# Performance work log

Measured on AMD Instinct MI355X. Metric: run time of the kernel, lower is better.

## Reference

```python
import jax, jax.numpy as jnp
import numpy as np

COORD = 5.0
NOOBJ = 0.5


def _reflat(x):
    # torch: flatten(x.transpose(0,1), start_dim=1).transpose(0,1) -> [B*S*S, C]
    C = x.shape[1]
    return jnp.moveaxis(x, 1, -1).reshape(-1, C)


def setup_inputs() -> dict:
    key = jax.random.key(0)
    k1, k2 = jax.random.split(key)
    B, C, S = 256, 25, 64
    inp = jax.random.uniform(k1, (B, C, S, S), dtype=jnp.float32)
    tgt = jax.random.uniform(k2, (B, C, S, S), dtype=jnp.float32)
    return {"input": inp, "target": tgt}


def _iou(b1, b2, blocks):
    # vectorized, detached IoU between predicted and target boxes, per row
    b1 = jax.lax.stop_gradient(b1)
    b2 = jax.lax.stop_gradient(b2)
    c1 = b1[:, :2] / blocks
    c2 = b2[:, :2] / blocks
    x1a, x2a = c1[:, 0] - b1[:, 2] / 2, c1[:, 0] + b1[:, 2] / 2
    y1a, y2a = c1[:, 1] - b1[:, 3] / 2, c1[:, 1] + b1[:, 3] / 2
    x1b, x2b = c2[:, 0] - b2[:, 2] / 2, c2[:, 0] + b2[:, 2] / 2
    y1b, y2b = c2[:, 1] - b2[:, 3] / 2, c2[:, 1] + b2[:, 3] / 2
    dx = jnp.minimum(x2a, x2b) - jnp.maximum(x1a, x1b)
    dy = jnp.minimum(y2a, y2b) - jnp.maximum(y1a, y1b)
    inter = dx * dy
    union = b1[:, 2] * b1[:, 3] + b2[:, 2] * b2[:, 3] - inter
    pos = (dx > 0) & (dy > 0)
    return jnp.where(pos, inter / jnp.where(pos, union, 1.0), 0.0)


def reference(input, target):
    blocks = target.shape[-1]
    t = _reflat(target)  # [N, C]
    p = _reflat(input)   # [N, C]
    m = (t[:, 4] > 0).astype(p.dtype)  # responsible-cell mask [N]
    iou = _iou(p[:, :4], t[:, :4], blocks)  # detached target confidence
    sp = jnp.sqrt(p[:, 2:4])
    st = jnp.sqrt(t[:, 2:4])
    m2 = m[:, None]
    loss = COORD * jnp.sum(m2 * jnp.square(p[:, :2] - t[:, :2]))
    loss += COORD * jnp.sum(m2 * jnp.square(sp - st))
    loss += jnp.sum(m * jnp.square(p[:, 4] - iou))
    loss += NOOBJ * jnp.sum((1.0 - m) * jnp.square(p[:, 4]))
    loss += jnp.sum(m2 * jnp.square(p[:, 5:] - t[:, 5:]))
    return loss
```

## Files before the change

### kernel.cpp

```cpp
#include <hip/hip_runtime.h>


#define COORD 5.0f
#define NOOBJ 0.5f

constexpr int B = 256;
constexpr int C = 25;
constexpr int S = 64;
constexpr int SS = S * S;
constexpr int CH_STRIDE4 = SS / 4;
constexpr int IMG_STRIDE4 = C * CH_STRIDE4;
constexpr int N4 = B * SS / 4;

__device__ __forceinline__ float comp(const float4 v, int k) {
    switch (k) {
        case 0: return v.x;
        case 1: return v.y;
        case 2: return v.z;
        default: return v.w;
    }
}

__global__ void zero_out_kernel(float* out) { out[0] = 0.0f; }

__global__ __launch_bounds__(256) void yolo_loss_kernel(
        const float4* __restrict__ in, const float4* __restrict__ tg,
        float* __restrict__ out) {
    const int g = blockIdx.x * blockDim.x + threadIdx.x;
    float acc = 0.0f;
    if (g < N4) {
        const int b = g >> 10;
        const int pp = g & 1023;
        const int base = b * IMG_STRIDE4 + pp;

        float4 p0 = in[base + 0 * CH_STRIDE4];
        float4 p1 = in[base + 1 * CH_STRIDE4];
        float4 p2 = in[base + 2 * CH_STRIDE4];
        float4 p3 = in[base + 3 * CH_STRIDE4];
        float4 p4 = in[base + 4 * CH_STRIDE4];
        float4 t0 = tg[base + 0 * CH_STRIDE4];
        float4 t1 = tg[base + 1 * CH_STRIDE4];
        float4 t2 = tg[base + 2 * CH_STRIDE4];
        float4 t3 = tg[base + 3 * CH_STRIDE4];
        float4 t4 = tg[base + 4 * CH_STRIDE4];

        float mv[4];
        const float invBlocks = 1.0f / (float)S;

        #pragma unroll
        for (int k = 0; k < 4; ++k) {
            const float px = comp(p0, k), py = comp(p1, k);
            const float pw = comp(p2, k), ph = comp(p3, k);
            const float pc = comp(p4, k);
            const float tx = comp(t0, k), ty = comp(t1, k);
            const float tw = comp(t2, k), th = comp(t3, k);
            const float tc = comp(t4, k);
            const float m = (tc > 0.0f) ? 1.0f : 0.0f;
            mv[k] = m;

            const float c1x = px * invBlocks, c1y = py * invBlocks;
            const float c2x = tx * invBlocks, c2y = ty * invBlocks;
            const float x1a = c1x - pw * 0.5f, x2a = c1x + pw * 0.5f;
            const float y1a = c1y - ph * 0.5f, y2a = c1y + ph * 0.5f;
            const float x1b = c2x - tw * 0.5f, x2b = c2x + tw * 0.5f;
            const float y1b = c2y - th * 0.5f, y2b = c2y + th * 0.5f;
            const float dx = fminf(x2a, x2b) - fmaxf(x1a, x1b);
            const float dy = fminf(y2a, y2b) - fmaxf(y1a, y1b);
            const float inter = dx * dy;
            const float uni = pw * ph + tw * th - inter;
            const bool pos = (dx > 0.0f) && (dy > 0.0f);
            const float iou = pos ? (inter / uni) : 0.0f;

            const float ex = px - tx, ey = py - ty;
            acc += COORD * m * (ex * ex + ey * ey);
            const float sw = sqrtf(pw) - sqrtf(tw);
            const float sh = sqrtf(ph) - sqrtf(th);
            acc += COORD * m * (sw * sw + sh * sh);
            const float ec = pc - iou;
            acc += m * ec * ec;
            acc += NOOBJ * (1.0f - m) * (pc * pc);
        }

        #pragma unroll
        for (int c = 5; c < 25; ++c) {
            const float4 pv = in[base + c * CH_STRIDE4];
            const float4 tv = tg[base + c * CH_STRIDE4];
            float d;
            d = pv.x - tv.x; acc += mv[0] * d * d;
            d = pv.y - tv.y; acc += mv[1] * d * d;
            d = pv.z - tv.z; acc += mv[2] * d * d;
            d = pv.w - tv.w; acc += mv[3] * d * d;
        }
    }

    #pragma unroll
    for (int off = 32; off > 0; off >>= 1)
        acc += __shfl_down(acc, off, 64);

    __shared__ float smem[4];
    const int lane = threadIdx.x & 63;
    const int wid = threadIdx.x >> 6;
    if (lane == 0) smem[wid] = acc;
    __syncthreads();
    if (threadIdx.x == 0) {
        const float s = smem[0] + smem[1] + smem[2] + smem[3];
        atomicAdd(out, s);
    }
}

extern "C" void kernel_launch(void* const* d_in, const int* in_sizes, int n_in,
                              void* d_out, int out_size, void* d_ws, size_t ws_size,
                              hipStream_t stream) {
    const float4* in = (const float4*)d_in[0];
    const float4* tg = (const float4*)d_in[1];
    float* out = (float*)d_out;

    zero_out_kernel<<<1, 1, 0, stream>>>(out);

    const int threads = 256;
    const int blocks = (N4 + threads - 1) / threads;
    yolo_loss_kernel<<<blocks, threads, 0, stream>>>(in, tg, out);
}
```

Before: 223.6 us.

## Split class-channel loss and box loss across separate block groups

Reorganizes the single kernel so 2560 blocks handle the 20 class channels as a flat grid-strided stream and the remaining blocks compute the box/IoU/confidence terms per cell. The aim is more parallelism and balanced memory streams instead of each thread serially loading all 25 channels. In exchange, class blocks re-read the target confidence channel once per class item, adding extra (mostly cached) traffic and index arithmetic.

```diff
diff --git a/kernel.cpp b/kernel.cpp
--- a/kernel.cpp
+++ b/kernel.cpp
@@ -11,6 +11,15 @@
 constexpr int CH_STRIDE4 = SS / 4;
 constexpr int IMG_STRIDE4 = C * CH_STRIDE4;
 constexpr int N4 = B * SS / 4;
+
+constexpr int THREADS = 256;
+constexpr int CLASS_CH = 20;
+constexpr int CLASS_ITEMS = CLASS_CH * N4;
+constexpr int CLASS_BLOCKS = 2560;
+constexpr int CLASS_THREADS = CLASS_BLOCKS * THREADS;
+constexpr int CLASS_IPT = CLASS_ITEMS / CLASS_THREADS;
+constexpr int BOX_BLOCKS = N4 / THREADS;
+constexpr int TOTAL_BLOCKS = CLASS_BLOCKS + BOX_BLOCKS;
 
 __device__ __forceinline__ float comp(const float4 v, int k) {
     switch (k) {
@@ -26,27 +35,52 @@
 __global__ __launch_bounds__(256) void yolo_loss_kernel(
         const float4* __restrict__ in, const float4* __restrict__ tg,
         float* __restrict__ out) {
-    const int g = blockIdx.x * blockDim.x + threadIdx.x;
     float acc = 0.0f;
-    if (g < N4) {
-        const int b = g >> 10;
-        const int pp = g & 1023;
-        const int base = b * IMG_STRIDE4 + pp;
 
-        float4 p0 = in[base + 0 * CH_STRIDE4];
-        float4 p1 = in[base + 1 * CH_STRIDE4];
-        float4 p2 = in[base + 2 * CH_STRIDE4];
-        float4 p3 = in[base + 3 * CH_STRIDE4];
-        float4 p4 = in[base + 4 * CH_STRIDE4];
-        float4 t0 = tg[base + 0 * CH_STRIDE4];
-        float4 t1 = tg[base + 1 * CH_STRIDE4];
-        float4 t2 = tg[base + 2 * CH_STRIDE4];
-        float4 t3 = tg[base + 3 * CH_STRIDE4];
-        float4 t4 = tg[base + 4 * CH_STRIDE4];
+    if (blockIdx.x < CLASS_BLOCKS) {
+        const int t = blockIdx.x * THREADS + threadIdx.x;
+        #pragma unroll
+        for (int i = 0; i < CLASS_IPT; i += 2) {
+            const int it0 = t + (i + 0) * CLASS_THREADS;
+            const int it1 = t + (i + 1) * CLASS_THREADS;
+            const int c0 = 5 + (it0 >> 18);
+            const int c1 = 5 + (it1 >> 18);
+            const int g0 = it0 & (N4 - 1);
+            const int g1 = it1 & (N4 - 1);
+            const int base0 = (g0 >> 10) * IMG_STRIDE4 + (g0 & 1023);
+            const int base1 = (g1 >> 10) * IMG_STRIDE4 + (g1 & 1023);
+            const float4 pv0 = in[base0 + c0 * CH_STRIDE4];
+            const float4 tv0 = tg[base0 + c0 * CH_STRIDE4];
+            const float4 mk0 = tg[base0 + 4 * CH_STRIDE4];
+            const float4 pv1 = in[base1 + c1 * CH_STRIDE4];
+            const float4 tv1 = tg[base1 + c1 * CH_STRIDE4];
+            const float4 mk1 = tg[base1 + 4 * CH_STRIDE4];
+            float d;
+            d = pv0.x - tv0.x; acc += (mk0.x > 0.0f) ? d * d : 0.0f;
+            d = pv0.y - tv0.y; acc += (mk0.y > 0.0f) ? d * d : 0.0f;
+            d = pv0.z - tv0.z; acc += (mk0.z > 0.0f) ? d * d : 0.0f;
+            d = pv0.w - tv0.w; acc += (mk0.w > 0.0f) ? d * d : 0.0f;
+            d = pv1.x - tv1.x; acc += (mk1.x > 0.0f) ? d * d : 0.0f;
+            d = pv1.y - tv1.y; acc += (mk1.y > 0.0f) ? d * d : 0.0f;
+            d = pv1.z - tv1.z; acc += (mk1.z > 0.0f) ? d * d : 0.0f;
+            d = pv1.w - tv1.w; acc += (mk1.w > 0.0f) ? d * d : 0.0f;
+        }
+    } else {
+        const int g = (blockIdx.x - CLASS_BLOCKS) * THREADS + threadIdx.x;
+        const int base = (g >> 10) * IMG_STRIDE4 + (g & 1023);
 
-        float mv[4];
+        const float4 p0 = in[base + 0 * CH_STRIDE4];
+        const float4 p1 = in[base + 1 * CH_STRIDE4];
+        const float4 p2 = in[base + 2 * CH_STRIDE4];
+        const float4 p3 = in[base + 3 * CH_STRIDE4];
+        const float4 p4 = in[base + 4 * CH_STRIDE4];
+        const float4 t0 = tg[base + 0 * CH_STRIDE4];
+        const float4 t1 = tg[base + 1 * CH_STRIDE4];
+        const float4 t2 = tg[base + 2 * CH_STRIDE4];
+        const float4 t3 = tg[base + 3 * CH_STRIDE4];
+        const float4 t4 = tg[base + 4 * CH_STRIDE4];
+
         const float invBlocks = 1.0f / (float)S;
-
         #pragma unroll
         for (int k = 0; k < 4; ++k) {
             const float px = comp(p0, k), py = comp(p1, k);
@@ -56,7 +90,6 @@
             const float tw = comp(t2, k), th = comp(t3, k);
             const float tc = comp(t4, k);
             const float m = (tc > 0.0f) ? 1.0f : 0.0f;
-            mv[k] = m;
 
             const float c1x = px * invBlocks, c1y = py * invBlocks;
             const float c2x = tx * invBlocks, c2y = ty * invBlocks;
@@ -79,17 +112,6 @@
             const float ec = pc - iou;
             acc += m * ec * ec;
             acc += NOOBJ * (1.0f - m) * (pc * pc);
-        }
-
-        #pragma unroll
-        for (int c = 5; c < 25; ++c) {
-            const float4 pv = in[base + c * CH_STRIDE4];
-            const float4 tv = tg[base + c * CH_STRIDE4];
-            float d;
-            d = pv.x - tv.x; acc += mv[0] * d * d;
-            d = pv.y - tv.y; acc += mv[1] * d * d;
-            d = pv.z - tv.z; acc += mv[2] * d * d;
-            d = pv.w - tv.w; acc += mv[3] * d * d;
         }
     }
 
@@ -117,7 +139,5 @@
 
     zero_out_kernel<<<1, 1, 0, stream>>>(out);
 
-    const int threads = 256;
-    const int blocks = (N4 + threads - 1) / threads;
-    yolo_loss_kernel<<<blocks, threads, 0, stream>>>(in, tg, out);
+    yolo_loss_kernel<<<TOTAL_BLOCKS, THREADS, 0, stream>>>(in, tg, out);
 }
```

Result: no change. 227.6 us (+1.8%).

## Split loss into separate class and box kernels with software-pipelined loads

Applied to the files above, without the earlier changes.

Replaces the single fused kernel with two kernels. A class kernel splits the 20 class channels into two halves of 10 across twice as many threads, with staged loads and sched barriers so loads overlap the FMA work. A box kernel handles two cells' box and IoU terms per thread. The aim is more memory-level parallelism and a better load schedule for this bandwidth-bound reduction. In exchange there is an extra kernel launch, the class kernel re-reads the confidence channel, and there are more atomics.

```diff
diff --git a/kernel.cpp b/kernel.cpp
--- a/kernel.cpp
+++ b/kernel.cpp
@@ -12,6 +12,11 @@
 constexpr int IMG_STRIDE4 = C * CH_STRIDE4;
 constexpr int N4 = B * SS / 4;
 
+constexpr int THREADS = 256;
+constexpr int CLASS_T_TOT = 2 * N4;
+constexpr int CLASS_BLOCKS = CLASS_T_TOT / THREADS;
+constexpr int BOX_BLOCKS = (N4 / 2) / THREADS;
+
 __device__ __forceinline__ float comp(const float4 v, int k) {
     switch (k) {
         case 0: return v.x;
@@ -21,91 +26,157 @@
     }
 }
 
-__global__ void zero_out_kernel(float* out) { out[0] = 0.0f; }
-
-__global__ __launch_bounds__(256) void yolo_loss_kernel(
-        const float4* __restrict__ in, const float4* __restrict__ tg,
-        float* __restrict__ out) {
-    const int g = blockIdx.x * blockDim.x + threadIdx.x;
-    float acc = 0.0f;
-    if (g < N4) {
-        const int b = g >> 10;
-        const int pp = g & 1023;
-        const int base = b * IMG_STRIDE4 + pp;
-
-        float4 p0 = in[base + 0 * CH_STRIDE4];
-        float4 p1 = in[base + 1 * CH_STRIDE4];
-        float4 p2 = in[base + 2 * CH_STRIDE4];
-        float4 p3 = in[base + 3 * CH_STRIDE4];
-        float4 p4 = in[base + 4 * CH_STRIDE4];
-        float4 t0 = tg[base + 0 * CH_STRIDE4];
-        float4 t1 = tg[base + 1 * CH_STRIDE4];
-        float4 t2 = tg[base + 2 * CH_STRIDE4];
-        float4 t3 = tg[base + 3 * CH_STRIDE4];
-        float4 t4 = tg[base + 4 * CH_STRIDE4];
-
-        float mv[4];
-        const float invBlocks = 1.0f / (float)S;
-
-        #pragma unroll
-        for (int k = 0; k < 4; ++k) {
-            const float px = comp(p0, k), py = comp(p1, k);
-            const float pw = comp(p2, k), ph = comp(p3, k);
-            const float pc = comp(p4, k);
-            const float tx = comp(t0, k), ty = comp(t1, k);
-            const float tw = comp(t2, k), th = comp(t3, k);
-            const float tc = comp(t4, k);
-            const float m = (tc > 0.0f) ? 1.0f : 0.0f;
-            mv[k] = m;
-
-            const float c1x = px * invBlocks, c1y = py * invBlocks;
-            const float c2x = tx * invBlocks, c2y = ty * invBlocks;
-            const float x1a = c1x - pw * 0.5f, x2a = c1x + pw * 0.5f;
-            const float y1a = c1y - ph * 0.5f, y2a = c1y + ph * 0.5f;
-            const float x1b = c2x - tw * 0.5f, x2b = c2x + tw * 0.5f;
-            const float y1b = c2y - th * 0.5f, y2b = c2y + th * 0.5f;
-            const float dx = fminf(x2a, x2b) - fmaxf(x1a, x1b);
-            const float dy = fminf(y2a, y2b) - fmaxf(y1a, y1b);
-            const float inter = dx * dy;
-            const float uni = pw * ph + tw * th - inter;
-            const bool pos = (dx > 0.0f) && (dy > 0.0f);
-            const float iou = pos ? (inter / uni) : 0.0f;
-
-            const float ex = px - tx, ey = py - ty;
-            acc += COORD * m * (ex * ex + ey * ey);
-            const float sw = sqrtf(pw) - sqrtf(tw);
-            const float sh = sqrtf(ph) - sqrtf(th);
-            acc += COORD * m * (sw * sw + sh * sh);
-            const float ec = pc - iou;
-            acc += m * ec * ec;
-            acc += NOOBJ * (1.0f - m) * (pc * pc);
-        }
-
-        #pragma unroll
-        for (int c = 5; c < 25; ++c) {
-            const float4 pv = in[base + c * CH_STRIDE4];
-            const float4 tv = tg[base + c * CH_STRIDE4];
-            float d;
-            d = pv.x - tv.x; acc += mv[0] * d * d;
-            d = pv.y - tv.y; acc += mv[1] * d * d;
-            d = pv.z - tv.z; acc += mv[2] * d * d;
-            d = pv.w - tv.w; acc += mv[3] * d * d;
-        }
-    }
-
+__device__ __forceinline__ void block_reduce_atomic(float acc, float* out) {
     #pragma unroll
     for (int off = 32; off > 0; off >>= 1)
         acc += __shfl_down(acc, off, 64);
-
     __shared__ float smem[4];
     const int lane = threadIdx.x & 63;
     const int wid = threadIdx.x >> 6;
     if (lane == 0) smem[wid] = acc;
     __syncthreads();
     if (threadIdx.x == 0) {
-        const float s = smem[0] + smem[1] + smem[2] + smem[3];
-        atomicAdd(out, s);
+        atomicAdd(out, smem[0] + smem[1] + smem[2] + smem[3]);
     }
+}
+
+__global__ void zero_out_kernel(float* out) { out[0] = 0.0f; }
+
+__device__ __forceinline__ void sq8(const float4 p0, const float4 t0,
+                                    const float4 p1, const float4 t1,
+                                    float mx, float my, float mz, float mw,
+                                    float& acc) {
+    float d;
+    d = p0.x - t0.x; acc = fmaf(mx * d, d, acc);
+    d = p0.y - t0.y; acc = fmaf(my * d, d, acc);
+    d = p0.z - t0.z; acc = fmaf(mz * d, d, acc);
+    d = p0.w - t0.w; acc = fmaf(mw * d, d, acc);
+    d = p1.x - t1.x; acc = fmaf(mx * d, d, acc);
+    d = p1.y - t1.y; acc = fmaf(my * d, d, acc);
+    d = p1.z - t1.z; acc = fmaf(mz * d, d, acc);
+    d = p1.w - t1.w; acc = fmaf(mw * d, d, acc);
+}
+
+__global__ __launch_bounds__(256, 4) void class_kernel(
+        const float4* __restrict__ in, const float4* __restrict__ tg,
+        float* __restrict__ out) {
+    const int T = blockIdx.x * THREADS + threadIdx.x;
+    const int g = T & (N4 - 1);
+    const int half = T >> 18;
+    const int base = (g >> 10) * IMG_STRIDE4 + (g & 1023);
+    const int c0 = 5 + half * 10;
+    const float4* inp = in + base + c0 * CH_STRIDE4;
+    const float4* tgp = tg + base + c0 * CH_STRIDE4;
+
+    const float4 t4 = tg[base + 4 * CH_STRIDE4];
+
+    float4 pA0 = inp[0 * 1024], tA0 = tgp[0 * 1024];
+    float4 pA1 = inp[1 * 1024], tA1 = tgp[1 * 1024];
+    float4 pB0 = inp[2 * 1024], tB0 = tgp[2 * 1024];
+    float4 pB1 = inp[3 * 1024], tB1 = tgp[3 * 1024];
+    float4 pC0 = inp[4 * 1024], tC0 = tgp[4 * 1024];
+    float4 pC1 = inp[5 * 1024], tC1 = tgp[5 * 1024];
+    __builtin_amdgcn_sched_barrier(0);
+
+    const float mx = t4.x > 0.0f ? 1.0f : 0.0f;
+    const float my = t4.y > 0.0f ? 1.0f : 0.0f;
+    const float mz = t4.z > 0.0f ? 1.0f : 0.0f;
+    const float mw = t4.w > 0.0f ? 1.0f : 0.0f;
+
+    float acc = 0.0f;
+
+    sq8(pA0, tA0, pA1, tA1, mx, my, mz, mw, acc);
+    pA0 = inp[6 * 1024]; tA0 = tgp[6 * 1024];
+    pA1 = inp[7 * 1024]; tA1 = tgp[7 * 1024];
+    __builtin_amdgcn_sched_barrier(0);
+
+    sq8(pB0, tB0, pB1, tB1, mx, my, mz, mw, acc);
+    pB0 = inp[8 * 1024]; tB0 = tgp[8 * 1024];
+    pB1 = inp[9 * 1024]; tB1 = tgp[9 * 1024];
+    __builtin_amdgcn_sched_barrier(0);
+
+    sq8(pC0, tC0, pC1, tC1, mx, my, mz, mw, acc);
+    sq8(pA0, tA0, pA1, tA1, mx, my, mz, mw, acc);
+    sq8(pB0, tB0, pB1, tB1, mx, my, mz, mw, acc);
+
+    block_reduce_atomic(acc, out);
+}
+
+__device__ __forceinline__ void boxAccum(
+        const float4 p0, const float4 p1, const float4 p2, const float4 p3,
+        const float4 p4, const float4 t0, const float4 t1, const float4 t2,
+        const float4 t3, const float4 t4, float& acc) {
+    const float invBlocks = 1.0f / (float)S;
+    #pragma unroll
+    for (int k = 0; k < 4; ++k) {
+        const float px = comp(p0, k), py = comp(p1, k);
+        const float pw = comp(p2, k), ph = comp(p3, k);
+        const float pc = comp(p4, k);
+        const float tx = comp(t0, k), ty = comp(t1, k);
+        const float tw = comp(t2, k), th = comp(t3, k);
+        const float tc = comp(t4, k);
+        const float m = (tc > 0.0f) ? 1.0f : 0.0f;
+
+        const float c1x = px * invBlocks, c1y = py * invBlocks;
+        const float c2x = tx * invBlocks, c2y = ty * invBlocks;
+        const float x1a = c1x - pw * 0.5f, x2a = c1x + pw * 0.5f;
+        const float y1a = c1y - ph * 0.5f, y2a = c1y + ph * 0.5f;
+        const float x1b = c2x - tw * 0.5f, x2b = c2x + tw * 0.5f;
+        const float y1b = c2y - th * 0.5f, y2b = c2y + th * 0.5f;
+        const float dx = fminf(x2a, x2b) - fmaxf(x1a, x1b);
+        const float dy = fminf(y2a, y2b) - fmaxf(y1a, y1b);
+        const float inter = dx * dy;
+        const float uni = pw * ph + tw * th - inter;
+        const bool pos = (dx > 0.0f) && (dy > 0.0f);
+        const float iou = pos ? (inter / uni) : 0.0f;
+
+        const float ex = px - tx, ey = py - ty;
+        acc += COORD * m * (ex * ex + ey * ey);
+        const float sw = sqrtf(pw) - sqrtf(tw);
+        const float sh = sqrtf(ph) - sqrtf(th);
+        acc += COORD * m * (sw * sw + sh * sh);
+        const float ec = pc - iou;
+        acc += m * ec * ec;
+        acc += NOOBJ * (1.0f - m) * (pc * pc);
+    }
+}
+
+__global__ __launch_bounds__(256, 2) void box_kernel(
+        const float4* __restrict__ in, const float4* __restrict__ tg,
+        float* __restrict__ out) {
+    const int tid = blockIdx.x * THREADS + threadIdx.x;
+    const int g0 = tid;
+    const int g1 = tid + N4 / 2;
+    const int b0 = (g0 >> 10) * IMG_STRIDE4 + (g0 & 1023);
+    const int b1 = (g1 >> 10) * IMG_STRIDE4 + (g1 & 1023);
+
+    const float4 ap0 = in[b0 + 0 * CH_STRIDE4];
+    const float4 ap1 = in[b0 + 1 * CH_STRIDE4];
+    const float4 ap2 = in[b0 + 2 * CH_STRIDE4];
+    const float4 ap3 = in[b0 + 3 * CH_STRIDE4];
+    const float4 ap4 = in[b0 + 4 * CH_STRIDE4];
+    const float4 at0 = tg[b0 + 0 * CH_STRIDE4];
+    const float4 at1 = tg[b0 + 1 * CH_STRIDE4];
+    const float4 at2 = tg[b0 + 2 * CH_STRIDE4];
+    const float4 at3 = tg[b0 + 3 * CH_STRIDE4];
+    const float4 at4 = tg[b0 + 4 * CH_STRIDE4];
+    const float4 bp0 = in[b1 + 0 * CH_STRIDE4];
+    const float4 bp1 = in[b1 + 1 * CH_STRIDE4];
+    const float4 bp2 = in[b1 + 2 * CH_STRIDE4];
+    const float4 bp3 = in[b1 + 3 * CH_STRIDE4];
+    const float4 bp4 = in[b1 + 4 * CH_STRIDE4];
+    const float4 bt0 = tg[b1 + 0 * CH_STRIDE4];
+    const float4 bt1 = tg[b1 + 1 * CH_STRIDE4];
+    const float4 bt2 = tg[b1 + 2 * CH_STRIDE4];
+    const float4 bt3 = tg[b1 + 3 * CH_STRIDE4];
+    const float4 bt4 = tg[b1 + 4 * CH_STRIDE4];
+    __builtin_amdgcn_sched_barrier(0);
+
+    float acc = 0.0f;
+    boxAccum(ap0, ap1, ap2, ap3, ap4, at0, at1, at2, at3, at4, acc);
+    boxAccum(bp0, bp1, bp2, bp3, bp4, bt0, bt1, bt2, bt3, bt4, acc);
+
+    block_reduce_atomic(acc, out);
 }
 
 extern "C" void kernel_launch(void* const* d_in, const int* in_sizes, int n_in,
@@ -117,7 +188,6 @@
 
     zero_out_kernel<<<1, 1, 0, stream>>>(out);
 
-    const int threads = 256;
-    const int blocks = (N4 + threads - 1) / threads;
-    yolo_loss_kernel<<<blocks, threads, 0, stream>>>(in, tg, out);
+    class_kernel<<<CLASS_BLOCKS, THREADS, 0, stream>>>(in, tg, out);
+    box_kernel<<<BOX_BLOCKS, THREADS, 0, stream>>>(in, tg, out);
 }
```

Measured after the change: 228.0 us. About the same (+2.0%).
